# Kernel tuning notes

Hardware: AMD Instinct MI355X
Metric: run time of the kernel (lower is better)

The kernel has to match this reference:

```python
import jax, jax.numpy as jnp
import numpy as np
import math

B, S, D = 4, 2048, 1024
H, DH = 16, 64  # num_heads, head dim (hardcoded 64 in module)


def setup_inputs() -> dict:
    key = jax.random.key(0)
    ks = jax.random.split(key, 5)
    scale = 0.02
    return {
        "x": jax.random.normal(ks[0], (B, S, D), dtype=jnp.float32),
        "W_Q": jax.random.normal(ks[1], (D, H * DH), dtype=jnp.float32) * scale,
        "W_K": jax.random.normal(ks[2], (D, H * DH), dtype=jnp.float32) * scale,
        "W_V": jax.random.normal(ks[3], (D, H * DH), dtype=jnp.float32) * scale,
        "W_O": jax.random.normal(ks[4], (H * DH, D), dtype=jnp.float32) * scale,
        "ln_gamma": jnp.ones((D,), dtype=jnp.float32),
        "ln_beta": jnp.zeros((D,), dtype=jnp.float32),
    }


def reference(x, W_Q, W_K, W_V, W_O, ln_gamma, ln_beta):
    # QKV projections (bias=False Linear: x @ W)
    q = (x @ W_Q).reshape(B, S, H, DH).transpose(0, 2, 1, 3)  # [B,H,S,DH]
    k = (x @ W_K).reshape(B, S, H, DH).transpose(0, 2, 1, 3)
    v = (x @ W_V).reshape(B, S, H, DH).transpose(0, 2, 1, 3)

    # scaled scores with causal mask (upper triangle, diag=1 -> -1e7)
    scores = jnp.einsum("bhsd,bhtd->bhst", q, k) / math.sqrt(DH)  # [B,H,S,S]
    causal = jnp.triu(jnp.ones((S, S), dtype=bool), k=1)
    scores = jnp.where(causal, jnp.float32(-1e7), scores)
    attn = jax.nn.softmax(scores, axis=-1)
    ctx = jnp.einsum("bhst,bhtd->bhsd", attn, v)  # [B,H,S,DH]

    # merge heads, output proj, residual, LayerNorm
    out = ctx.transpose(0, 2, 1, 3).reshape(B, S, H * DH) @ W_O + x
    mu = jnp.mean(out, axis=-1, keepdims=True)
    var = jnp.mean((out - mu) ** 2, axis=-1, keepdims=True)
    out = (out - mu) * jax.lax.rsqrt(var + 1e-5) * ln_gamma + ln_beta
    return out
```

## Files before the change

### kernel.cpp

```cpp
#include <hip/hip_runtime.h>
#include <hip/hip_bf16.h>
#include <cstdint>
#include <cstddef>

#define S_ 2048
#define D_ 1024
#define H_ 16
#define DH_ 64
#define M_ 8192

using bf16 = __bf16;
using bf16x4 = __attribute__((ext_vector_type(4))) __bf16;
using bf16x8 = __attribute__((ext_vector_type(8))) __bf16;
using f32x4 = __attribute__((ext_vector_type(4))) float;
using s16x4 = __attribute__((ext_vector_type(4))) short;

__device__ __forceinline__ void g2lds16(const bf16* g, bf16* l) {
  __builtin_amdgcn_global_load_lds(
      (const __attribute__((address_space(1))) void*)g,
      (__attribute__((address_space(3))) void*)l, 16, 0, 0);
}

__device__ __forceinline__ f32x4 mfma16(bf16x4 a, bf16x4 b, f32x4 c) {
#if __has_builtin(__builtin_amdgcn_mfma_f32_16x16x16_bf16)
  return __builtin_amdgcn_mfma_f32_16x16x16_bf16(a, b, c, 0, 0, 0);
#elif __has_builtin(__builtin_amdgcn_mfma_f32_16x16x16bf16_1k)
  return __builtin_amdgcn_mfma_f32_16x16x16bf16_1k(
      __builtin_bit_cast(s16x4, a), __builtin_bit_cast(s16x4, b), c, 0, 0, 0);
#else
  f32x4 d;
  asm("v_mfma_f32_16x16x16_bf16 %0, %1, %2, %3"
      : "=v"(d)
      : "v"(a), "v"(b), "v"(c));
  return d;
#endif
}

__global__ __launch_bounds__(256) void cvt_all_kernel(
    const float* __restrict__ x, const float* __restrict__ w0,
    const float* __restrict__ w1, const float* __restrict__ w2,
    const float* __restrict__ w3, bf16* __restrict__ xb,
    bf16* __restrict__ o0, bf16* __restrict__ o1, bf16* __restrict__ o2,
    bf16* __restrict__ o3) {
  __shared__ float tile[32][33];
  int bx = blockIdx.x;
  int tid = threadIdx.x;
  if (bx < 4096) {
    size_t i = ((size_t)bx * 256 + tid) * 8;
    float4 a = *(const float4*)(x + i);
    float4 b = *(const float4*)(x + i + 4);
    bf16x8 o;
    o[0] = (bf16)a.x; o[1] = (bf16)a.y; o[2] = (bf16)a.z; o[3] = (bf16)a.w;
    o[4] = (bf16)b.x; o[5] = (bf16)b.y; o[6] = (bf16)b.z; o[7] = (bf16)b.w;
    *(bf16x8*)(xb + i) = o;
    return;
  }
  int wb = bx - 4096;
  int wsel = wb >> 10; wb &= 1023;
  const float* W; bf16* O;
  switch (wsel) {
    case 0: W = w0; O = o0; break;
    case 1: W = w1; O = o1; break;
    case 2: W = w2; O = o2; break;
    default: W = w3; O = o3; break;
  }
  int n0 = (wb & 31) * 32;
  int k0 = (wb >> 5) * 32;
#pragma unroll
  for (int i = 0; i < 4; ++i) {
    int e = tid + i * 256; int rr = e >> 5, cc = e & 31;
    tile[rr][cc] = W[(size_t)(k0 + rr) * 1024 + n0 + cc];
  }
  __syncthreads();
#pragma unroll
  for (int i = 0; i < 4; ++i) {
    int e = tid + i * 256; int rr = e >> 5, cc = e & 31;
    O[(size_t)(n0 + rr) * 1024 + k0 + cc] = (bf16)tile[cc][rr];
  }
}

template <int MODE>
__global__ __launch_bounds__(512, 2) void gemm_kernel(
    const bf16* __restrict__ A,
    const bf16* __restrict__ Bt0, const bf16* __restrict__ Bt1,
    const bf16* __restrict__ Bt2,
    bf16* __restrict__ Qo, bf16* __restrict__ Ko, bf16* __restrict__ Vto,
    const float* __restrict__ xres, float* __restrict__ out) {
  extern __shared__ float4 smem4[];
  bf16* smem = (bf16*)smem4;

  constexpr int NWG = (MODE == 0) ? 768 : 256;
  constexpr int CPX = NWG / 8;
  constexpr int NBN = (MODE == 0) ? 12 : 4;
  const int wg = ((int)blockIdx.x & 7) * CPX + ((int)blockIdx.x >> 3);
  const int bn = wg % NBN, bm = wg / NBN;

  const bf16* Bt;
  int n0full = 0, wsel = 0;
  if constexpr (MODE == 0) {
    wsel = bn >> 2;
    Bt = (wsel == 0) ? Bt0 : (wsel == 1 ? Bt1 : Bt2);
    n0full = (bn & 3) * 256;
  } else {
    Bt = Bt0;
    n0full = bn * 256;
  }

  const int tid = threadIdx.x;
  const int wave = tid >> 6, lane = tid & 63;
  const int quad = lane >> 4, r = lane & 15;
  const int wm = (wave >> 2) * 64, wn = (wave & 3) * 64;

  const int lrow = lane >> 3;
  const int lcol = ((lane & 7) ^ lrow) * 8;
  const int am0 = bm * 128 + wave * 8 + lrow;
  const int am1 = am0 + 64;
  const bf16 *p0, *p1, *p2, *p3, *p4, *p5;
  if constexpr (MODE == 0) {
    p0 = A + (size_t)am0 * 1024 + lcol;
    p1 = A + (size_t)am1 * 1024 + lcol;
  } else {
    p0 = A + (size_t)(am0 >> 11) * (16 * (size_t)S_ * DH_) +
         (size_t)(am0 & 2047) * 64 + lcol;
    p1 = A + (size_t)(am1 >> 11) * (16 * (size_t)S_ * DH_) +
         (size_t)(am1 & 2047) * 64 + lcol;
  }
  const int bnr = n0full + wave * 8 + lrow;
  p2 = Bt + (size_t)bnr * 1024 + lcol;
  p3 = Bt + (size_t)(bnr + 64) * 1024 + lcol;
  p4 = Bt + (size_t)(bnr + 128) * 1024 + lcol;
  p5 = Bt + (size_t)(bnr + 192) * 1024 + lcol;
  constexpr ptrdiff_t dA = (MODE == 0) ? 64 : (ptrdiff_t)S_ * DH_;

  const int oA0 = wave * 512, oA1 = (8 + wave) * 512;
  const int oB0 = 8192 + wave * 512, oB1 = 8192 + (8 + wave) * 512;
  const int oB2 = 8192 + (16 + wave) * 512, oB3 = 8192 + (24 + wave) * 512;

  auto stage = [&](bf16* base) {
    g2lds16(p0, base + oA0); p0 += dA;
    g2lds16(p1, base + oA1); p1 += dA;
    g2lds16(p2, base + oB0); p2 += 64;
    g2lds16(p3, base + oB1); p3 += 64;
    g2lds16(p4, base + oB2); p4 += 64;
    g2lds16(p5, base + oB3); p5 += 64;
  };

  f32x4 acc[4][4];
  const f32x4 zero = {0.f, 0.f, 0.f, 0.f};
#pragma unroll
  for (int i = 0; i < 4; ++i)
#pragma unroll
    for (int j = 0; j < 4; ++j) acc[i][j] = zero;

  const int rw = r & 7;
  const int x0 = (quad ^ rw) * 8;
  const int x1 = ((quad + 4) ^ rw) * 8;
  const int raB = (wm + r) * 64;
  const int rbB = (wn + r) * 64;

  auto phases = [&](const bf16* buf) {
    const bf16* bA = buf;
    const bf16* bB = buf + 8192;
    bf16x8 af[4], bg[4];
#pragma unroll
    for (int i = 0; i < 4; ++i)
      af[i] = *(const bf16x8*)(bA + raB + i * 1024 + x0);
#pragma unroll
    for (int j = 0; j < 4; ++j)
      bg[j] = *(const bf16x8*)(bB + rbB + j * 1024 + x0);
    __builtin_amdgcn_s_setprio(1);
#pragma unroll
    for (int i = 0; i < 4; ++i)
#pragma unroll
      for (int j = 0; j < 4; ++j)
        acc[i][j] = __builtin_amdgcn_mfma_f32_16x16x32_bf16(af[i], bg[j],
                                                            acc[i][j], 0, 0, 0);
    __builtin_amdgcn_s_setprio(0);
#pragma unroll
    for (int i = 0; i < 4; ++i)
      af[i] = *(const bf16x8*)(bA + raB + i * 1024 + x1);
#pragma unroll
    for (int j = 0; j < 4; ++j)
      bg[j] = *(const bf16x8*)(bB + rbB + j * 1024 + x1);
    __builtin_amdgcn_s_setprio(1);
#pragma unroll
    for (int i = 0; i < 4; ++i)
#pragma unroll
      for (int j = 0; j < 4; ++j)
        acc[i][j] = __builtin_amdgcn_mfma_f32_16x16x32_bf16(af[i], bg[j],
                                                            acc[i][j], 0, 0, 0);
    __builtin_amdgcn_s_setprio(0);
  };

  bf16* b0 = smem;
  bf16* b1 = smem + 24576;
  bf16* b2 = smem + 49152;

  stage(b0);
  stage(b1);

#pragma unroll 1
  for (int kt = 0; kt < 15; kt += 3) {
    asm volatile("s_waitcnt vmcnt(6)\n\ts_barrier" ::: "memory");
    stage(b2);
    phases(b0);
    asm volatile("s_waitcnt vmcnt(6)\n\ts_barrier" ::: "memory");
    stage(b0);
    phases(b1);
    asm volatile("s_waitcnt vmcnt(6)\n\ts_barrier" ::: "memory");
    if (kt < 12) stage(b1);
    phases(b2);
  }
  asm volatile("s_waitcnt vmcnt(0)\n\ts_barrier" ::: "memory");
  phases(b0);

  const int mB = bm * 128 + wm + quad * 4;
  if constexpr (MODE == 0) {
    if (wsel < 2) {
      bf16* dst = (wsel == 0) ? Qo : Ko;
#pragma unroll
      for (int i = 0; i < 4; ++i) {
#pragma unroll
        for (int j = 0; j < 4; ++j) {
          int n = n0full + wn + j * 16 + r;
          int h = n >> 6, dh = n & 63;
#pragma unroll
          for (int g = 0; g < 4; ++g) {
            int m = mB + i * 16 + g;
            int b = m >> 11, s = m & 2047;
            dst[((size_t)(b * H_ + h) * S_ + s) * DH_ + dh] =
                (bf16)acc[i][j][g];
          }
        }
      }
    } else {
#pragma unroll
      for (int i = 0; i < 4; ++i) {
        int m = mB + i * 16;
        int b = m >> 11, s = m & 2047;
#pragma unroll
        for (int j = 0; j < 4; ++j) {
          int n = n0full + wn + j * 16 + r;
          int h = n >> 6, dh = n & 63;
          bf16x4 pk;
#pragma unroll
          for (int g = 0; g < 4; ++g) pk[g] = (bf16)acc[i][j][g];
          *(bf16x4*)(Vto + ((size_t)(b * H_ + h) * DH_ + dh) * S_ + s) = pk;
        }
      }
    }
  } else {
#pragma unroll
    for (int i = 0; i < 4; ++i) {
#pragma unroll
      for (int j = 0; j < 4; ++j) {
        int n = bn * 256 + wn + j * 16 + r;
#pragma unroll
        for (int g = 0; g < 4; ++g) {
          int m = mB + i * 16 + g;
          size_t idx = (size_t)m * 1024 + n;
          out[idx] = acc[i][j][g] + xres[idx];
        }
      }
    }
  }
}

__global__ __launch_bounds__(512, 4) void attn_kernel(const bf16* __restrict__ Qb,
                                                      const bf16* __restrict__ Kb,
                                                      const bf16* __restrict__ Vtb,
                                                      bf16* __restrict__ ctx) {
  __shared__ __align__(16) bf16 smK[2][2][64 * 64];
  __shared__ __align__(16) bf16 smV[2][2][64 * 64];
  const int bx = blockIdx.x;
  const int bh = bx & 63;
  const int i256 = (bx < 256) ? (7 - (bx >> 6)) : ((bx - 256) >> 6);
  const bf16* Qh = Qb + (size_t)bh * S_ * DH_;
  const bf16* Kh = Kb + (size_t)bh * S_ * DH_;
  const bf16* Vh = Vtb + (size_t)bh * DH_ * S_;
  bf16* Ch = ctx + (size_t)bh * S_ * DH_;
  const int tid = threadIdx.x, wave = tid >> 6, lane = tid & 63;
  const int quad = lane >> 4, r = lane & 15;
  const int r7 = r & 7;
  const int wrow = wave * 8 + (lane >> 3);
  const int gcol = ((lane & 7) ^ (lane >> 3)) * 8;
  const f32x4 zero = {0.f, 0.f, 0.f, 0.f};
  const int xk0 = (quad ^ r7) * 8, xk1 = ((quad + 4) ^ r7) * 8;

  const int q0w = i256 * 256 + wave * 32;
  const int numkt = 4 * i256 + 4;
  const int NU = numkt >> 1;
  const int lastkt = q0w >> 6;

  bf16x8 qf[2][2];
  const float qsc = 0.125f * 1.44269504f;
#pragma unroll
  for (int qg = 0; qg < 2; ++qg)
#pragma unroll
    for (int hh = 0; hh < 2; ++hh) {
      bf16x8 q = *(const bf16x8*)(Qh + (size_t)(q0w + qg * 16 + r) * DH_ +
                                  hh * 32 + quad * 8);
#pragma unroll
      for (int i = 0; i < 8; ++i) q[i] = (bf16)((float)q[i] * qsc);
      qf[qg][hh] = q;
    }

  f32x4 lacc[2] = {zero, zero};
  f32x4 oacc[2][4];
#pragma unroll
  for (int qg = 0; qg < 2; ++qg)
#pragma unroll
    for (int tn = 0; tn < 4; ++tn) oacc[qg][tn] = zero;

  auto STAGE = [&](int u, int b) {
#pragma unroll
    for (int sub = 0; sub < 2; ++sub) {
      const int kt = 2 * u + sub;
      g2lds16(Kh + (size_t)(kt * 64 + wrow) * DH_ + gcol,
              &smK[b][sub][wave * 512]);
      g2lds16(Vh + (size_t)wrow * S_ + kt * 64 + gcol,
              &smV[b][sub][wave * 512]);
    }
  };

  STAGE(0, 0);
  asm volatile("s_waitcnt vmcnt(0)\n\ts_barrier" ::: "memory");

#pragma unroll 1
  for (int u = 0; u < NU; ++u) {
    const int b = u & 1;
    if (u + 1 < NU) STAGE(u + 1, b ^ 1);
#pragma unroll
    for (int sub = 0; sub < 2; ++sub) {
      const int kt = 2 * u + sub;
      if (kt <= lastkt) {
        const int kv0 = kt * 64;
        const bf16* kb = &smK[b][sub][0];
        const bf16* vb = &smV[b][sub][0];

        f32x4 s[2][4];
#pragma unroll
        for (int t = 0; t < 4; ++t) {
          bf16x8 kf0 = *(const bf16x8*)(kb + (t * 16 + r) * 64 + xk0);
          bf16x8 kf1 = *(const bf16x8*)(kb + (t * 16 + r) * 64 + xk1);
#pragma unroll
          for (int qg = 0; qg < 2; ++qg) {
            f32x4 z = __builtin_amdgcn_mfma_f32_16x16x32_bf16(kf0, qf[qg][0],
                                                              zero, 0, 0, 0);
            s[qg][t] = __builtin_amdgcn_mfma_f32_16x16x32_bf16(kf1, qf[qg][1],
                                                               z, 0, 0, 0);
          }
        }
        if (kt == lastkt) {
#pragma unroll
          for (int qg = 0; qg < 2; ++qg) {
            const int q = q0w + qg * 16 + r;
#pragma unroll
            for (int t = 0; t < 4; ++t) {
              const int kv = kv0 + t * 16 + quad * 4;
#pragma unroll
              for (int g = 0; g < 4; ++g)
                if (kv + g > q) s[qg][t][g] = -1e30f;
            }
          }
        }
#pragma unroll
        for (int t = 0; t < 4; ++t) {
          bf16x4 pa[2];
#pragma unroll
          for (int qg = 0; qg < 2; ++qg) {
#pragma unroll
            for (int g = 0; g < 4; ++g)
              s[qg][t][g] = __builtin_amdgcn_exp2f(s[qg][t][g]);
            lacc[qg] += s[qg][t];
            bf16x4 pk;
#pragma unroll
            for (int g = 0; g < 4; ++g) pk[g] = (bf16)s[qg][t][g];
            pa[qg] = pk;
          }
#pragma unroll
          for (int tn = 0; tn < 4; ++tn) {
            bf16x4 vf = *(const bf16x4*)(
                vb + (tn * 16 + r) * 64 +
                ((2 * t + (quad >> 1)) ^ r7) * 8 + (quad & 1) * 4);
            oacc[0][tn] = mfma16(pa[0], vf, oacc[0][tn]);
            oacc[1][tn] = mfma16(pa[1], vf, oacc[1][tn]);
          }
        }
      }
    }
    asm volatile("s_waitcnt vmcnt(0) lgkmcnt(0)\n\ts_barrier" ::: "memory");
  }

#pragma unroll
  for (int qg = 0; qg < 2; ++qg) {
    float rs = (lacc[qg][0] + lacc[qg][1]) + (lacc[qg][2] + lacc[qg][3]);
    rs += __shfl_xor(rs, 16, 64);
    rs += __shfl_xor(rs, 32, 64);
    const float inv = 1.f / rs;
    f32x4 ib;
#pragma unroll
    for (int g = 0; g < 4; ++g) ib[g] = __shfl(inv, quad * 4 + g, 64);
#pragma unroll
    for (int tn = 0; tn < 4; ++tn) {
      f32x4 ov = oacc[qg][tn] * ib;
#pragma unroll
      for (int g = 0; g < 4; ++g)
        Ch[(size_t)(q0w + qg * 16 + quad * 4 + g) * DH_ + tn * 16 + r] =
            (bf16)ov[g];
    }
  }
}

__global__ __launch_bounds__(256) void ln_kernel(float* __restrict__ out,
                                                 const float* __restrict__ gamma,
                                                 const float* __restrict__ beta) {
  __shared__ float red[8];
  size_t row = blockIdx.x;
  float* p = out + row * 1024;
  int tid = threadIdx.x;
  float4 v = ((const float4*)p)[tid];
  float s1 = v.x + v.y + v.z + v.w;
  float s2 = v.x * v.x + v.y * v.y + v.z * v.z + v.w * v.w;
#pragma unroll
  for (int o = 1; o < 64; o <<= 1) {
    s1 += __shfl_xor(s1, o, 64);
    s2 += __shfl_xor(s2, o, 64);
  }
  int wave = tid >> 6, lane = tid & 63;
  if (lane == 0) { red[wave] = s1; red[4 + wave] = s2; }
  __syncthreads();
  s1 = red[0] + red[1] + red[2] + red[3];
  s2 = red[4] + red[5] + red[6] + red[7];
  float mean = s1 * (1.f / 1024.f);
  float var = s2 * (1.f / 1024.f) - mean * mean;
  float rstd = rsqrtf(var + 1e-5f);
  float4 g = ((const float4*)gamma)[tid];
  float4 b = ((const float4*)beta)[tid];
  float4 o;
  o.x = (v.x - mean) * rstd * g.x + b.x;
  o.y = (v.y - mean) * rstd * g.y + b.y;
  o.z = (v.z - mean) * rstd * g.z + b.z;
  o.w = (v.w - mean) * rstd * g.w + b.w;
  ((float4*)p)[tid] = o;
}

extern "C" void kernel_launch(void* const* d_in, const int* in_sizes, int n_in,
                              void* d_out, int out_size, void* d_ws,
                              size_t ws_size, hipStream_t stream) {
  (void)in_sizes; (void)n_in; (void)out_size; (void)ws_size;
  const float* x  = (const float*)d_in[0];
  const float* WQ = (const float*)d_in[1];
  const float* WK = (const float*)d_in[2];
  const float* WV = (const float*)d_in[3];
  const float* WO = (const float*)d_in[4];
  const float* gamma = (const float*)d_in[5];
  const float* beta  = (const float*)d_in[6];
  float* out = (float*)d_out;

  bf16* ws = (bf16*)d_ws;
  const size_t MD = (size_t)M_ * D_;
  const size_t WW = (size_t)D_ * D_;
  bf16* xb   = ws;
  bf16* wqt  = xb + MD;
  bf16* wkt  = wqt + WW;
  bf16* wvt  = wkt + WW;
  bf16* wot  = wvt + WW;
  bf16* Qb   = wot + WW;
  bf16* Kb   = Qb + MD;
  bf16* Vtb  = Kb + MD;
  bf16* ctxb = Vtb + MD;

  constexpr int GEMM_LDS = 3 * 48 * 1024;
  static bool s_attr = false;
  if (!s_attr) {
    s_attr = true;
    (void)hipFuncSetAttribute(reinterpret_cast<const void*>(gemm_kernel<0>),
                              hipFuncAttributeMaxDynamicSharedMemorySize,
                              GEMM_LDS);
    (void)hipFuncSetAttribute(reinterpret_cast<const void*>(gemm_kernel<1>),
                              hipFuncAttributeMaxDynamicSharedMemorySize,
                              GEMM_LDS);
  }

  cvt_all_kernel<<<dim3(8192), dim3(256), 0, stream>>>(
      x, WQ, WK, WV, WO, xb, wqt, wkt, wvt, wot);
  gemm_kernel<0><<<dim3(768), dim3(512), GEMM_LDS, stream>>>(
      xb, wqt, wkt, wvt, Qb, Kb, Vtb, nullptr, nullptr);
  attn_kernel<<<dim3(512), dim3(512), 0, stream>>>(Qb, Kb, Vtb, ctxb);
  gemm_kernel<1><<<dim3(256), dim3(512), GEMM_LDS, stream>>>(
      ctxb, wot, nullptr, nullptr, nullptr, nullptr, nullptr, x, out);
  ln_kernel<<<dim3(8192), dim3(256), 0, stream>>>(out, gamma, beta);
}
```

Before: 254.3 us.

## Halve GEMM K-tile to 32 to shrink LDS and raise occupancy to four blocks

Reduces the GEMM K-step from 64 to 32, shrinking each of the three LDS buffers from 48 KB to 24 KB. Launch bounds change from 2 to 4 blocks per CU. The global-to-LDS staging is rewritten for the narrower tile: three 16-byte loads per thread with a new swizzle, and alternating A-pointer strides for the ctx layout. The pipelined loop runs twice as many iterations. The aim is better latency hiding through occupancy, at the cost of more barriers per unit of MFMA work and tighter register budgets.

```diff
diff --git a/kernel.cpp b/kernel.cpp
--- a/kernel.cpp
+++ b/kernel.cpp
@@ -80,7 +80,7 @@
 }
 
 template <int MODE>
-__global__ __launch_bounds__(512, 2) void gemm_kernel(
+__global__ __launch_bounds__(512, 4) void gemm_kernel(
     const bf16* __restrict__ A,
     const bf16* __restrict__ Bt0, const bf16* __restrict__ Bt1,
     const bf16* __restrict__ Bt2,
@@ -111,38 +111,32 @@
   const int quad = lane >> 4, r = lane & 15;
   const int wm = (wave >> 2) * 64, wn = (wave & 3) * 64;
 
-  const int lrow = lane >> 3;
-  const int lcol = ((lane & 7) ^ lrow) * 8;
-  const int am0 = bm * 128 + wave * 8 + lrow;
-  const int am1 = am0 + 64;
-  const bf16 *p0, *p1, *p2, *p3, *p4, *p5;
+  const int lrow = lane >> 2;
+  const int lcol = ((lane & 3) ^ (lrow & 3)) * 8;
+  const int am = bm * 128 + wave * 16 + lrow;
+  const bf16 *pA, *pB1, *pB2;
   if constexpr (MODE == 0) {
-    p0 = A + (size_t)am0 * 1024 + lcol;
-    p1 = A + (size_t)am1 * 1024 + lcol;
+    pA = A + (size_t)am * 1024 + lcol;
   } else {
-    p0 = A + (size_t)(am0 >> 11) * (16 * (size_t)S_ * DH_) +
-         (size_t)(am0 & 2047) * 64 + lcol;
-    p1 = A + (size_t)(am1 >> 11) * (16 * (size_t)S_ * DH_) +
-         (size_t)(am1 & 2047) * 64 + lcol;
-  }
-  const int bnr = n0full + wave * 8 + lrow;
-  p2 = Bt + (size_t)bnr * 1024 + lcol;
-  p3 = Bt + (size_t)(bnr + 64) * 1024 + lcol;
-  p4 = Bt + (size_t)(bnr + 128) * 1024 + lcol;
-  p5 = Bt + (size_t)(bnr + 192) * 1024 + lcol;
-  constexpr ptrdiff_t dA = (MODE == 0) ? 64 : (ptrdiff_t)S_ * DH_;
-
-  const int oA0 = wave * 512, oA1 = (8 + wave) * 512;
-  const int oB0 = 8192 + wave * 512, oB1 = 8192 + (8 + wave) * 512;
-  const int oB2 = 8192 + (16 + wave) * 512, oB3 = 8192 + (24 + wave) * 512;
+    pA = A + (size_t)(am >> 11) * (16 * (size_t)S_ * DH_) +
+         (size_t)(am & 2047) * 64 + lcol;
+  }
+  const int bnr = n0full + wave * 16 + lrow;
+  pB1 = Bt + (size_t)bnr * 1024 + lcol;
+  pB2 = Bt + (size_t)(bnr + 128) * 1024 + lcol;
+  constexpr ptrdiff_t dSum = (MODE == 0) ? 64 : (ptrdiff_t)S_ * DH_;
+  ptrdiff_t dTog = 32;
+
+  const int oA = wave * 512;
+  const int oB1 = 4096 + wave * 512;
+  const int oB2 = 8192 + wave * 512;
 
   auto stage = [&](bf16* base) {
-    g2lds16(p0, base + oA0); p0 += dA;
-    g2lds16(p1, base + oA1); p1 += dA;
-    g2lds16(p2, base + oB0); p2 += 64;
-    g2lds16(p3, base + oB1); p3 += 64;
-    g2lds16(p4, base + oB2); p4 += 64;
-    g2lds16(p5, base + oB3); p5 += 64;
+    g2lds16(pA, base + oA);
+    g2lds16(pB1, base + oB1);
+    g2lds16(pB2, base + oB2);
+    pA += dTog; dTog = dSum - dTog;
+    pB1 += 32; pB2 += 32;
   };
 
   f32x4 acc[4][4];
@@ -152,36 +146,20 @@
 #pragma unroll
     for (int j = 0; j < 4; ++j) acc[i][j] = zero;
 
-  const int rw = r & 7;
-  const int x0 = (quad ^ rw) * 8;
-  const int x1 = ((quad + 4) ^ rw) * 8;
-  const int raB = (wm + r) * 64;
-  const int rbB = (wn + r) * 64;
-
-  auto phases = [&](const bf16* buf) {
+  const int x0 = (quad ^ (r & 3)) * 8;
+  const int raB = (wm + r) * 32;
+  const int rbB = (wn + r) * 32;
+
+  auto phase = [&](const bf16* buf) {
     const bf16* bA = buf;
-    const bf16* bB = buf + 8192;
+    const bf16* bB = buf + 4096;
     bf16x8 af[4], bg[4];
 #pragma unroll
     for (int i = 0; i < 4; ++i)
-      af[i] = *(const bf16x8*)(bA + raB + i * 1024 + x0);
+      af[i] = *(const bf16x8*)(bA + raB + i * 512 + x0);
 #pragma unroll
     for (int j = 0; j < 4; ++j)
-      bg[j] = *(const bf16x8*)(bB + rbB + j * 1024 + x0);
-    __builtin_amdgcn_s_setprio(1);
-#pragma unroll
-    for (int i = 0; i < 4; ++i)
-#pragma unroll
-      for (int j = 0; j < 4; ++j)
-        acc[i][j] = __builtin_amdgcn_mfma_f32_16x16x32_bf16(af[i], bg[j],
-                                                            acc[i][j], 0, 0, 0);
-    __builtin_amdgcn_s_setprio(0);
-#pragma unroll
-    for (int i = 0; i < 4; ++i)
-      af[i] = *(const bf16x8*)(bA + raB + i * 1024 + x1);
-#pragma unroll
-    for (int j = 0; j < 4; ++j)
-      bg[j] = *(const bf16x8*)(bB + rbB + j * 1024 + x1);
+      bg[j] = *(const bf16x8*)(bB + rbB + j * 512 + x0);
     __builtin_amdgcn_s_setprio(1);
 #pragma unroll
     for (int i = 0; i < 4; ++i)
@@ -193,26 +171,28 @@
   };
 
   bf16* b0 = smem;
-  bf16* b1 = smem + 24576;
-  bf16* b2 = smem + 49152;
+  bf16* b1 = smem + 12288;
+  bf16* b2 = smem + 24576;
 
   stage(b0);
   stage(b1);
 
 #pragma unroll 1
-  for (int kt = 0; kt < 15; kt += 3) {
-    asm volatile("s_waitcnt vmcnt(6)\n\ts_barrier" ::: "memory");
+  for (int kt = 0; kt < 30; kt += 3) {
+    asm volatile("s_waitcnt vmcnt(3)\n\ts_barrier" ::: "memory");
     stage(b2);
-    phases(b0);
-    asm volatile("s_waitcnt vmcnt(6)\n\ts_barrier" ::: "memory");
+    phase(b0);
+    asm volatile("s_waitcnt vmcnt(3)\n\ts_barrier" ::: "memory");
     stage(b0);
-    phases(b1);
-    asm volatile("s_waitcnt vmcnt(6)\n\ts_barrier" ::: "memory");
-    if (kt < 12) stage(b1);
-    phases(b2);
-  }
+    phase(b1);
+    asm volatile("s_waitcnt vmcnt(3)\n\ts_barrier" ::: "memory");
+    stage(b1);
+    phase(b2);
+  }
+  asm volatile("s_waitcnt vmcnt(3)\n\ts_barrier" ::: "memory");
+  phase(b0);
   asm volatile("s_waitcnt vmcnt(0)\n\ts_barrier" ::: "memory");
-  phases(b0);
+  phase(b1);
 
   const int mB = bm * 128 + wm + quad * 4;
   if constexpr (MODE == 0) {
@@ -471,7 +451,7 @@
   bf16* Vtb  = Kb + MD;
   bf16* ctxb = Vtb + MD;
 
-  constexpr int GEMM_LDS = 3 * 48 * 1024;
+  constexpr int GEMM_LDS = 3 * 24 * 1024;
   static bool s_attr = false;
   if (!s_attr) {
     s_attr = true;
```

Result: faster. 248.7 us (-2.2%).
